# Kernel optimization log

Measured on AMD Instinct MI355X. Metric: run time of the kernel, lower is better.

## Reference

```python
import jax, jax.numpy as jnp
import numpy as np

N = 10000      # nodes
E = 320000     # edges (avg degree 32)
C = 256        # feature dim (input_dim == output_dim)
L = 3          # num_layers
D = 20         # KAF dictionary size
BOUNDARY = 4.0 # KAF dictionary boundary


def setup_inputs() -> dict:
    key = jax.random.key(0)
    ks = jax.random.split(key, 7)
    x = jax.random.normal(ks[0], (N, C), jnp.float32)
    edge_index = jax.random.randint(ks[1], (2, E), 0, N, jnp.int32)
    edge_attr = jax.random.normal(ks[2], (E, 2), jnp.float32)
    # per-layer stacked parameters (all layers have identical shapes)
    node_w = jax.random.normal(ks[3], (L, C, C), jnp.float32) / jnp.sqrt(jnp.float32(C))
    edge_w = jax.random.normal(ks[4], (L, 2, C), jnp.float32) / jnp.sqrt(jnp.float32(2))
    neigh_w = jax.random.normal(ks[5], (L, C, C), jnp.float32) / jnp.sqrt(jnp.float32(C))
    bias = jnp.zeros((L, C), jnp.float32)
    alpha = jax.random.normal(ks[6], (L, C, D), jnp.float32) * 0.3
    return dict(x=x, edge_index=edge_index, edge_attr=edge_attr,
                node_w=node_w, edge_w=edge_w, neigh_w=neigh_w, bias=bias, alpha=alpha)


def _kaf(s, alpha_l):
    # Kernel Activation Function (Scardapane et al.): per-channel Gaussian mixture
    dict_pts = jnp.linspace(-BOUNDARY, BOUNDARY, D, dtype=s.dtype)  # [D]
    interval = 2.0 * BOUNDARY / (D - 1)
    gamma = 0.5 / (2.0 * interval) ** 2
    K = jnp.exp(-gamma * jnp.square(s[..., None] - dict_pts))  # [N, C, D]
    return jnp.einsum('ncd,cd->nc', K, alpha_l)


def reference(x, edge_index, edge_attr, node_w, edge_w, neigh_w, bias, alpha):
    src, dst = edge_index[0], edge_index[1]
    # mean-aggregation normalizer (computed once; graph is fixed across layers)
    cnt = jax.ops.segment_sum(jnp.ones((E,), x.dtype), dst, num_segments=N)
    inv_cnt = jnp.where(cnt > 0, 1.0 / jnp.maximum(cnt, 1.0), 0.0)  # [N]
    h = x
    for l in range(L):
        # message: edge_attr @ W_e + x_j @ W_n  -> [E, C]
        msg = edge_attr @ edge_w[l] + h[src] @ neigh_w[l]
        # mean aggregate to destination nodes
        aggr = jax.ops.segment_sum(msg, dst, num_segments=N) * inv_cnt[:, None]
        # update: KAF(aggr + x @ W + b)
        h = _kaf(aggr + h @ node_w[l] + bias[l], alpha[l])
    return h
```

## Files before the change

### kernel.cpp

```cpp
#include <hip/hip_runtime.h>
#include <hip/hip_bf16.h>

#define N_NODES 10000
#define N_EDGES 320000
#define B_PRE   80
#define EPB     (N_EDGES / B_PRE)
#define SLK     130

typedef __attribute__((ext_vector_type(8))) _Float16 half8;
typedef __attribute__((ext_vector_type(4))) _Float16 half4;
typedef __attribute__((ext_vector_type(4))) float floatx4;

#define OFF_RS    0
#define OFF_INVC  40960
#define OFF_S2    81920
#define OFF_COLV  163840
#define OFF_WCAT  806912
#define OFF_HA    1593344
#define OFF_HB    6713344
#define OFF_G     11833344
#define OFF_PERC  OFF_G
#define OFF_BASE  (OFF_G + 1600000)
#define OFF_CTOT  (OFF_G + 4800000)

__global__ __launch_bounds__(1024) void k_prepc(const float4* __restrict__ x, half4* __restrict__ hA,
                                                const float* __restrict__ neigh_w, const float* __restrict__ node_w,
                                                _Float16* __restrict__ wcatT,
                                                const int* __restrict__ ei, const float* __restrict__ ea,
                                                unsigned short* __restrict__ percnt,
                                                float2* __restrict__ s2part) {
  __shared__ int hist[N_NODES];
  __shared__ float2 sxy[N_NODES];
  const int tid = threadIdx.x, b = blockIdx.x;

  if (b < B_PRE) {
    for (int n = tid; n < N_NODES; n += 1024) { hist[n] = 0; sxy[n] = make_float2(0.f, 0.f); }
    __syncthreads();
    const int e0 = b * EPB;
    for (int e = e0 + tid; e < e0 + EPB; e += 1024) {
      int d = ei[N_EDGES + e];
      float2 a = ((const float2*)ea)[e];
      atomicAdd(&hist[d], 1);
      atomicAdd(&sxy[d].x, a.x);
      atomicAdd(&sxy[d].y, a.y);
    }
    __syncthreads();
    for (int n = tid; n < N_NODES; n += 1024) {
      percnt[b * N_NODES + n] = (unsigned short)hist[n];
      s2part[b * N_NODES + n] = sxy[n];
    }
    return;
  }
  if (b < B_PRE + 384) {
    float (*t)[33] = (float(*)[33])hist;
    const int bb = b - B_PRE;
    const int k0 = (bb & 15) * 32;
    const int n0 = ((bb >> 4) & 7) * 32;
    const int l  = bb >> 7;
    const int r = tid >> 5, c = tid & 31;
    const float* src = (k0 < 256) ? neigh_w : node_w;
    const int kb = (k0 < 256) ? k0 : (k0 - 256);
    t[r][c] = src[l * 65536 + (kb + r) * 256 + (n0 + c)];
    __syncthreads();
    wcatT[(size_t)l * 131072 + (n0 + r) * 512 + (k0 + c)] = (_Float16)t[c][r];
    return;
  }
  int i = (b - (B_PRE + 384)) * 1024 + tid;
  float4 v = x[i];
  half4 h; h.x = (_Float16)v.x; h.y = (_Float16)v.y; h.z = (_Float16)v.z; h.w = (_Float16)v.w;
  hA[i] = h;
}

__global__ __launch_bounds__(256) void k_base(const unsigned short* __restrict__ percnt,
                                              const float2* __restrict__ s2part,
                                              int* __restrict__ prefix, int* __restrict__ cnttot,
                                              float* __restrict__ s2) {
  int n = blockIdx.x * 256 + threadIdx.x;
  if (n >= N_NODES) return;
  int s = 0;
  float sx = 0.f, sy = 0.f;
  for (int b = 0; b < B_PRE; ++b) {
    prefix[b * N_NODES + n] = s;
    s += (int)percnt[b * N_NODES + n];
    float2 p = s2part[b * N_NODES + n];
    sx += p.x; sy += p.y;
  }
  cnttot[n] = s;
  s2[2 * n] = sx; s2[2 * n + 1] = sy;
}

__global__ __launch_bounds__(1024) void k_scan(const int* __restrict__ cnttot,
                                               int* __restrict__ rs, float* __restrict__ invc) {
  __shared__ int lds[1024];
  const int t = threadIdx.x;
  const int base = t * 10;
  int loc[10];
  int sum = 0;
#pragma unroll
  for (int i = 0; i < 10; ++i) {
    int idx = base + i;
    int v = (idx < N_NODES) ? cnttot[idx] : 0;
    loc[i] = v; sum += v;
  }
  lds[t] = sum; __syncthreads();
  for (int off = 1; off < 1024; off <<= 1) {
    int v = 0;
    if (t >= off) v = lds[t - off];
    __syncthreads();
    if (t >= off) lds[t] += v;
    __syncthreads();
  }
  int ex = lds[t] - sum;
#pragma unroll
  for (int i = 0; i < 10; ++i) {
    int idx = base + i;
    if (idx < N_NODES) {
      rs[idx] = ex; ex += loc[i];
      invc[idx] = (loc[i] > 0) ? (1.0f / (float)loc[i]) : 0.0f;
    }
  }
  if (t == 1023) rs[N_NODES] = lds[1023];
}

__global__ __launch_bounds__(1024) void k_scat(const int* __restrict__ ei,
                                               const int* __restrict__ prefix, const int* __restrict__ rs,
                                               unsigned short* __restrict__ colv) {
  __shared__ int cur[N_NODES];
  const int t = threadIdx.x, b = blockIdx.x;
  for (int n = t; n < N_NODES; n += 1024)
    cur[n] = rs[n] + prefix[b * N_NODES + n];
  __syncthreads();
  const int e0 = b * EPB;
  for (int e = e0 + t; e < e0 + EPB; e += 1024) {
    int d = ei[N_EDGES + e];
    int src = ei[e];
    int pos = atomicAdd(&cur[d], 1);
    colv[pos] = (unsigned short)src;
  }
}

__global__ __launch_bounds__(256) void k_aggr(const int* __restrict__ rs, const unsigned short* __restrict__ colv,
                                              const float* __restrict__ invc,
                                              const _Float16* __restrict__ H, _Float16* __restrict__ Gm) {
  const int wv   = threadIdx.x >> 6;
  const int lane = threadIdx.x & 63;
  const int hf   = lane >> 5;
  const int l5   = lane & 31;
  const int n = blockIdx.x * 4 + wv;
  int beg = rs[n], end = rs[n + 1];
  beg = max(0, min(beg, N_EDGES));
  end = max(beg, min(end, N_EDGES));
  const int co = l5 * 8;

  half8 a0 = (half8)(_Float16)0.f, a1 = (half8)(_Float16)0.f;
  half8 a2 = (half8)(_Float16)0.f, a3 = (half8)(_Float16)0.f;
  half8 a4 = (half8)(_Float16)0.f, a5 = (half8)(_Float16)0.f;
  half8 a6 = (half8)(_Float16)0.f, a7 = (half8)(_Float16)0.f;
  for (int base = beg; base < end; base += 64) {
    const int cnt = min(64, end - base);
    int myIdx = 0;
    if (base + lane < end) myIdx = (int)colv[base + lane];
    int j = 0;
    for (; j + 16 <= cnt; j += 16) {
      int s[8];
#pragma unroll
      for (int k = 0; k < 8; ++k) s[k] = __shfl(myIdx, j + 2 * k + hf);
      half8 v[8];
#pragma unroll
      for (int k = 0; k < 8; ++k) v[k] = *(const half8*)(H + (size_t)s[k] * 256 + co);
      a0 += v[0]; a1 += v[1]; a2 += v[2]; a3 += v[3];
      a4 += v[4]; a5 += v[5]; a6 += v[6]; a7 += v[7];
    }
    for (; j + 8 <= cnt; j += 8) {
      int s0 = __shfl(myIdx, j + hf);
      int s1 = __shfl(myIdx, j + 2 + hf);
      int s2i = __shfl(myIdx, j + 4 + hf);
      int s3 = __shfl(myIdx, j + 6 + hf);
      half8 v0 = *(const half8*)(H + (size_t)s0 * 256 + co);
      half8 v1 = *(const half8*)(H + (size_t)s1 * 256 + co);
      half8 v2 = *(const half8*)(H + (size_t)s2i * 256 + co);
      half8 v3 = *(const half8*)(H + (size_t)s3 * 256 + co);
      a0 += v0; a1 += v1; a2 += v2; a3 += v3;
    }
    for (; j + 2 <= cnt; j += 2) {
      int s0 = __shfl(myIdx, j + hf);
      a0 += *(const half8*)(H + (size_t)s0 * 256 + co);
    }
    if (j < cnt) {
      int s0 = __shfl(myIdx, j);
      if (hf == 0)
        a0 += *(const half8*)(H + (size_t)s0 * 256 + co);
    }
  }
  half8 acc0 = ((a0 + a4) + (a1 + a5)) + ((a2 + a6) + (a3 + a7));
  union { half8 h; unsigned int u[4]; } me, ot;
  me.h = acc0;
#pragma unroll
  for (int r = 0; r < 4; ++r) ot.u[r] = (unsigned int)__shfl_xor((int)me.u[r], 32);
  acc0 = me.h + ot.h;

  if (hf == 0) {
    const float ic = invc[n];
    half8 o;
#pragma unroll
    for (int k = 0; k < 8; ++k) o[k] = (_Float16)((float)acc0[k] * ic);
    *(half8*)(Gm + (size_t)n * 256 + co) = o;
  }
}

__global__ __launch_bounds__(256) void k_gemm2(const _Float16* __restrict__ Gm,
                                               const _Float16* __restrict__ Hm,
                                               const _Float16* __restrict__ BT,
                                               const float* __restrict__ ew,
                                               const float* __restrict__ bias,
                                               const float* __restrict__ alpha,
                                               const float* __restrict__ invc,
                                               const float* __restrict__ s2,
                                               _Float16* __restrict__ hout, float* __restrict__ fout,
                                               int final_layer) {
  __shared__ _Float16 As[64 * SLK];
  __shared__ _Float16 Bs[64 * SLK];
  __shared__ float alds[64 * 20];
  const int tid = threadIdx.x;
  const int wv = tid >> 6;
  const int lane = tid & 63;
  const int m0 = blockIdx.x * 64;
  const int n0 = blockIdx.y * 64;
  const int wy = wv >> 1, wx = wv & 1;

#pragma unroll
  for (int ii = 0; ii < 5; ++ii)
    alds[tid + 256 * ii] = alpha[n0 * 20 + tid + 256 * ii];

  floatx4 acc[2][2];
#pragma unroll
  for (int i = 0; i < 2; ++i)
#pragma unroll
    for (int j = 0; j < 2; ++j) acc[i][j] = (floatx4){0.f, 0.f, 0.f, 0.f};

  const int mrow = 32 * wy + (lane & 15);
  const int nrow = 32 * wx + (lane & 15);
  const int q8 = (lane >> 4) * 8;

#pragma unroll
  for (int kt = 0; kt < 4; ++kt) {
    const _Float16* Asrc = (kt < 2) ? Gm : Hm;
    const int ko = (kt & 1) * 128;
    half8 av[4], bv[4];
#pragma unroll
    for (int c = 0; c < 4; ++c) {
      int ch = tid + 256 * c;
      int row = ch >> 4;
      int off = (ch & 15) * 8;
      int arow = m0 + row; if (arow >= N_NODES) arow = N_NODES - 1;
      av[c] = *(const half8*)(Asrc + (size_t)arow * 256 + ko + off);
      bv[c] = *(const half8*)(BT + (size_t)(n0 + row) * 512 + kt * 128 + off);
    }
    __syncthreads();
#pragma unroll
    for (int c = 0; c < 4; ++c) {
      int ch = tid + 256 * c;
      int row = ch >> 4;
      int off = (ch & 15) * 8;
      *(half8*)&As[row * SLK + off] = av[c];
      *(half8*)&Bs[row * SLK + off] = bv[c];
    }
    __syncthreads();
#pragma unroll
    for (int ks = 0; ks < 4; ++ks) {
      const int kb = ks * 32 + q8;
      half8 af0 = *(const half8*)&As[mrow * SLK + kb];
      half8 af1 = *(const half8*)&As[(mrow + 16) * SLK + kb];
      half8 bf0 = *(const half8*)&Bs[nrow * SLK + kb];
      half8 bf1 = *(const half8*)&Bs[(nrow + 16) * SLK + kb];
      acc[0][0] = __builtin_amdgcn_mfma_f32_16x16x32_f16(af0, bf0, acc[0][0], 0, 0, 0);
      acc[0][1] = __builtin_amdgcn_mfma_f32_16x16x32_f16(af0, bf1, acc[0][1], 0, 0, 0);
      acc[1][0] = __builtin_amdgcn_mfma_f32_16x16x32_f16(af1, bf0, acc[1][0], 0, 0, 0);
      acc[1][1] = __builtin_amdgcn_mfma_f32_16x16x32_f16(af1, bf1, acc[1][1], 0, 0, 0);
    }
  }

  const int rowb = m0 + 32 * wy + 4 * (lane >> 4);
  const int clb  = 32 * wx + (lane & 15);
  float icr[2][4], t0r[2][4], t1r[2][4];
#pragma unroll
  for (int i = 0; i < 2; ++i)
#pragma unroll
    for (int r = 0; r < 4; ++r) {
      int rw = rowb + 16 * i + r;
      int rc = (rw < N_NODES) ? rw : (N_NODES - 1);
      icr[i][r] = invc[rc];
      t0r[i][r] = s2[2 * rc];
      t1r[i][r] = s2[2 * rc + 1];
    }
  const float WM = 0.7788007831f;
#pragma unroll
  for (int j = 0; j < 2; ++j) {
    const int cl = clb + 16 * j;
    const int cn = n0 + cl;
    const float e0 = ew[cn], e1 = ew[256 + cn], bi = bias[cn];
    float a20[20];
#pragma unroll
    for (int q = 0; q < 5; ++q)
      *(float4*)&a20[4 * q] = *(const float4*)&alds[cl * 20 + 4 * q];
#pragma unroll
    for (int i = 0; i < 2; ++i) {
      float K[4], R[4], o[4];
#pragma unroll
      for (int r = 0; r < 4; ++r) {
        float sv = acc[i][j][r] + icr[i][r] * (t0r[i][r] * e0 + t1r[i][r] * e1) + bi;
        float tt = fminf(fmaxf(sv, -40.f), 40.f);
        float dd = tt + 4.0f;
        K[r] = __expf(-0.705078125f * dd * dd);
        R[r] = __expf(0.59375f * dd - 0.125f);
        o[r] = 0.f;
      }
#pragma unroll
      for (int d = 0; d < 20; ++d) {
        o[0] += a20[d] * K[0]; K[0] *= R[0]; R[0] *= WM;
        o[1] += a20[d] * K[1]; K[1] *= R[1]; R[1] *= WM;
        o[2] += a20[d] * K[2]; K[2] *= R[2]; R[2] *= WM;
        o[3] += a20[d] * K[3]; K[3] *= R[3]; R[3] *= WM;
      }
      const int rw0 = rowb + 16 * i;
      if (final_layer) {
#pragma unroll
        for (int r = 0; r < 4; ++r)
          if (rw0 + r < N_NODES) fout[(size_t)(rw0 + r) * 256 + cn] = o[r];
      } else {
#pragma unroll
        for (int r = 0; r < 4; ++r)
          if (rw0 + r < N_NODES) hout[(size_t)(rw0 + r) * 256 + cn] = (_Float16)o[r];
      }
    }
  }
}

extern "C" void kernel_launch(void* const* d_in, const int* in_sizes, int n_in,
                              void* d_out, int out_size, void* d_ws, size_t ws_size,
                              hipStream_t stream) {
  const float* x       = (const float*)d_in[0];
  const int*   ei      = (const int*)d_in[1];
  const float* ea      = (const float*)d_in[2];
  const float* node_w  = (const float*)d_in[3];
  const float* edge_w  = (const float*)d_in[4];
  const float* neigh_w = (const float*)d_in[5];
  const float* bias    = (const float*)d_in[6];
  const float* alpha   = (const float*)d_in[7];

  char* w = (char*)d_ws;
  int*            rs     = (int*)(w + OFF_RS);
  float*          invc   = (float*)(w + OFF_INVC);
  float*          s2     = (float*)(w + OFF_S2);
  unsigned short* colv   = (unsigned short*)(w + OFF_COLV);
  _Float16*       wcatT  = (_Float16*)(w + OFF_WCAT);
  _Float16*       hA     = (_Float16*)(w + OFF_HA);
  _Float16*       hB     = (_Float16*)(w + OFF_HB);
  _Float16*       g      = (_Float16*)(w + OFF_G);
  unsigned short* percnt = (unsigned short*)(w + OFF_PERC);
  int*            prefix = (int*)(w + OFF_BASE);
  int*            cnttot = (int*)(w + OFF_CTOT);
  float*          fout   = (float*)d_out;
  float2*         s2part = (float2*)d_out;

  k_prepc<<<B_PRE + 384 + 625, 1024, 0, stream>>>((const float4*)x, (half4*)hA,
                                                  neigh_w, node_w, wcatT, ei, ea, percnt, s2part);
  k_base<<<40, 256, 0, stream>>>(percnt, s2part, prefix, cnttot, s2);
  k_scan<<<1, 1024, 0, stream>>>(cnttot, rs, invc);
  k_scat<<<B_PRE, 1024, 0, stream>>>(ei, prefix, rs, colv);

  _Float16* hin = hA;
  for (int l = 0; l < 3; ++l) {
    k_aggr<<<2500, 256, 0, stream>>>(rs, colv, invc, hin, g);
    _Float16* hout = (l == 0) ? hB : hA;
    k_gemm2<<<dim3(157, 4), 256, 0, stream>>>(g, hin, wcatT + (size_t)l * 131072,
                                              edge_w + l * 512, bias + l * 256, alpha + l * 5120,
                                              invc, s2, hout, fout, (l == 2) ? 1 : 0);
    hin = hout;
  }
}
```

Before: 208.4 us.

## Fuse count scan into base kernel via last-block ticket, split edge-attr sums

Merges the single-block exclusive scan into the per-node prefix kernel. The last of 40 blocks, picked by an atomic ticket counter, runs a 256-thread scan, which removes one kernel launch. The per-block edge-attr partial sums are split into separate x and y float arrays. The y sum is accumulated in a second LDS pass so LDS holds one float array instead of a float2 array, and the reduction over the 80 partials moves into 40 extra blocks. This risks extra LDS passes in the preprocessing blocks and a serial 40-element loop per scan thread.

```diff
diff --git a/kernel.cpp b/kernel.cpp
--- a/kernel.cpp
+++ b/kernel.cpp
@@ -22,33 +22,45 @@
 #define OFF_PERC  OFF_G
 #define OFF_BASE  (OFF_G + 1600000)
 #define OFF_CTOT  (OFF_G + 4800000)
+#define OFF_TICK  (OFF_G + 4840960)
 
 __global__ __launch_bounds__(1024) void k_prepc(const float4* __restrict__ x, half4* __restrict__ hA,
                                                 const float* __restrict__ neigh_w, const float* __restrict__ node_w,
                                                 _Float16* __restrict__ wcatT,
                                                 const int* __restrict__ ei, const float* __restrict__ ea,
                                                 unsigned short* __restrict__ percnt,
-                                                float2* __restrict__ s2part) {
-  __shared__ int hist[N_NODES];
-  __shared__ float2 sxy[N_NODES];
+                                                float* __restrict__ s2px, float* __restrict__ s2py,
+                                                int* __restrict__ tick) {
+  __shared__ int   hist[N_NODES];
+  __shared__ float sfl[N_NODES];
   const int tid = threadIdx.x, b = blockIdx.x;
 
+  if (b == 0 && tid == 0) *tick = 0;
+
   if (b < B_PRE) {
-    for (int n = tid; n < N_NODES; n += 1024) { hist[n] = 0; sxy[n] = make_float2(0.f, 0.f); }
+    for (int n = tid; n < N_NODES; n += 1024) { hist[n] = 0; sfl[n] = 0.f; }
     __syncthreads();
     const int e0 = b * EPB;
+    int   dreg[4]; float ayreg[4]; int cnt = 0;
     for (int e = e0 + tid; e < e0 + EPB; e += 1024) {
       int d = ei[N_EDGES + e];
       float2 a = ((const float2*)ea)[e];
       atomicAdd(&hist[d], 1);
-      atomicAdd(&sxy[d].x, a.x);
-      atomicAdd(&sxy[d].y, a.y);
+      atomicAdd(&sfl[d], a.x);
+      dreg[cnt] = d; ayreg[cnt] = a.y; ++cnt;
     }
     __syncthreads();
     for (int n = tid; n < N_NODES; n += 1024) {
       percnt[b * N_NODES + n] = (unsigned short)hist[n];
-      s2part[b * N_NODES + n] = sxy[n];
-    }
+      s2px[b * N_NODES + n] = sfl[n];
+    }
+    __syncthreads();
+    for (int n = tid; n < N_NODES; n += 1024) sfl[n] = 0.f;
+    __syncthreads();
+    for (int i = 0; i < cnt; ++i) atomicAdd(&sfl[dreg[i]], ayreg[i]);
+    __syncthreads();
+    for (int n = tid; n < N_NODES; n += 1024)
+      s2py[b * N_NODES + n] = sfl[n];
     return;
   }
   if (b < B_PRE + 384) {
@@ -72,54 +84,68 @@
 }
 
 __global__ __launch_bounds__(256) void k_base(const unsigned short* __restrict__ percnt,
-                                              const float2* __restrict__ s2part,
+                                              const float* __restrict__ s2px, const float* __restrict__ s2py,
                                               int* __restrict__ prefix, int* __restrict__ cnttot,
-                                              float* __restrict__ s2) {
-  int n = blockIdx.x * 256 + threadIdx.x;
-  if (n >= N_NODES) return;
-  int s = 0;
-  float sx = 0.f, sy = 0.f;
-  for (int b = 0; b < B_PRE; ++b) {
-    prefix[b * N_NODES + n] = s;
-    s += (int)percnt[b * N_NODES + n];
-    float2 p = s2part[b * N_NODES + n];
-    sx += p.x; sy += p.y;
-  }
-  cnttot[n] = s;
-  s2[2 * n] = sx; s2[2 * n + 1] = sy;
-}
-
-__global__ __launch_bounds__(1024) void k_scan(const int* __restrict__ cnttot,
-                                               int* __restrict__ rs, float* __restrict__ invc) {
-  __shared__ int lds[1024];
-  const int t = threadIdx.x;
-  const int base = t * 10;
-  int loc[10];
+                                              int* __restrict__ rs, float* __restrict__ invc,
+                                              float* __restrict__ s2, int* __restrict__ tick) {
+  const int tid = threadIdx.x, b = blockIdx.x;
+  if (b >= 40) {
+    int n = (b - 40) * 256 + tid;
+    if (n >= N_NODES) return;
+    float sx = 0.f, sy = 0.f;
+    for (int bb = 0; bb < B_PRE; ++bb) {
+      sx += s2px[bb * N_NODES + n];
+      sy += s2py[bb * N_NODES + n];
+    }
+    s2[2 * n] = sx; s2[2 * n + 1] = sy;
+    return;
+  }
+  {
+    int n = b * 256 + tid;
+    if (n < N_NODES) {
+      int s = 0;
+      for (int bb = 0; bb < B_PRE; ++bb) {
+        prefix[bb * N_NODES + n] = s;
+        s += (int)percnt[bb * N_NODES + n];
+      }
+      cnttot[n] = s;
+    }
+  }
+  __shared__ int lastflag;
+  __threadfence();
+  if (tid == 0) lastflag = (atomicAdd(tick, 1) == 39);
+  __syncthreads();
+  if (!lastflag) return;
+  __threadfence();
+
+  __shared__ int slds[256];
+  const int base = tid * 40;
+  int loc[40];
   int sum = 0;
 #pragma unroll
-  for (int i = 0; i < 10; ++i) {
+  for (int i = 0; i < 40; ++i) {
     int idx = base + i;
     int v = (idx < N_NODES) ? cnttot[idx] : 0;
     loc[i] = v; sum += v;
   }
-  lds[t] = sum; __syncthreads();
-  for (int off = 1; off < 1024; off <<= 1) {
+  slds[tid] = sum; __syncthreads();
+  for (int off = 1; off < 256; off <<= 1) {
     int v = 0;
-    if (t >= off) v = lds[t - off];
-    __syncthreads();
-    if (t >= off) lds[t] += v;
-    __syncthreads();
-  }
-  int ex = lds[t] - sum;
-#pragma unroll
-  for (int i = 0; i < 10; ++i) {
+    if (tid >= off) v = slds[tid - off];
+    __syncthreads();
+    if (tid >= off) slds[tid] += v;
+    __syncthreads();
+  }
+  int ex = slds[tid] - sum;
+#pragma unroll
+  for (int i = 0; i < 40; ++i) {
     int idx = base + i;
     if (idx < N_NODES) {
       rs[idx] = ex; ex += loc[i];
       invc[idx] = (loc[i] > 0) ? (1.0f / (float)loc[i]) : 0.0f;
     }
   }
-  if (t == 1023) rs[N_NODES] = lds[1023];
+  if (tid == 255) rs[N_NODES] = slds[255];
 }
 
 __global__ __launch_bounds__(1024) void k_scat(const int* __restrict__ ei,
@@ -360,13 +386,15 @@
   unsigned short* percnt = (unsigned short*)(w + OFF_PERC);
   int*            prefix = (int*)(w + OFF_BASE);
   int*            cnttot = (int*)(w + OFF_CTOT);
+  int*            tick   = (int*)(w + OFF_TICK);
   float*          fout   = (float*)d_out;
-  float2*         s2part = (float2*)d_out;
+  float*          s2px   = (float*)d_out;
+  float*          s2py   = (float*)((char*)d_out + 3200000);
 
   k_prepc<<<B_PRE + 384 + 625, 1024, 0, stream>>>((const float4*)x, (half4*)hA,
-                                                  neigh_w, node_w, wcatT, ei, ea, percnt, s2part);
-  k_base<<<40, 256, 0, stream>>>(percnt, s2part, prefix, cnttot, s2);
-  k_scan<<<1, 1024, 0, stream>>>(cnttot, rs, invc);
+                                                  neigh_w, node_w, wcatT, ei, ea, percnt,
+                                                  s2px, s2py, tick);
+  k_base<<<80, 256, 0, stream>>>(percnt, s2px, s2py, prefix, cnttot, rs, invc, s2, tick);
   k_scat<<<B_PRE, 1024, 0, stream>>>(ei, prefix, rs, colv);
 
   _Float16* hin = hA;
```

Measured after the change: 220.4 us. +5.8%, slower.
